# Kernel optimization log

Hardware: AMD Instinct MI355X
Metric: run time of the kernel (lower is better)

## Reference

```python
import jax, jax.numpy as jnp
import numpy as np

H = 64      # hidden_size
IN = 3      # input_size (output_size + force dim)
OUT = 2     # output_size


def setup_inputs() -> dict:
    key = jax.random.key(0)
    ks = jax.random.split(key, 8)
    B, T, PL = 1024, 512, 300
    s = 1.0 / np.sqrt(H)  # pytorch default init range
    x = jax.random.normal(ks[0], (B, T, IN), jnp.float32)
    force = jax.random.normal(ks[1], (B, PL - 1, 1), jnp.float32)
    W_ih = jax.random.uniform(ks[2], (4 * H, IN), jnp.float32, -s, s)
    W_hh = jax.random.uniform(ks[3], (4 * H, H), jnp.float32, -s, s)
    b_ih = jax.random.uniform(ks[4], (4 * H,), jnp.float32, -s, s)
    b_hh = jax.random.uniform(ks[5], (4 * H,), jnp.float32, -s, s)
    W_out = jax.random.uniform(ks[6], (OUT, H), jnp.float32, -s, s)
    b_out = jax.random.uniform(ks[7], (OUT,), jnp.float32, -s, s)
    return {"x": x, "force": force, "W_ih": W_ih, "W_hh": W_hh,
            "b_ih": b_ih, "b_hh": b_hh, "W_out": W_out, "b_out": b_out,
            "predict_length": PL}


def _lstm_cell(h, c, x_t, W_ih, W_hh, b):
    # pytorch gate order: i, f, g, o
    g = x_t @ W_ih.T + h @ W_hh.T + b
    i, f, gg, o = jnp.split(g, 4, axis=-1)
    c_new = jax.nn.sigmoid(f) * c + jax.nn.sigmoid(i) * jnp.tanh(gg)
    h_new = jax.nn.sigmoid(o) * jnp.tanh(c_new)
    return h_new, c_new


def reference(x, force, W_ih, W_hh, b_ih, b_hh, W_out, b_out, predict_length):
    b = b_ih + b_hh
    B = x.shape[0]
    h0 = jnp.zeros((B, H), x.dtype)
    c0 = jnp.zeros((B, H), x.dtype)

    # ---- encoder: run LSTM over full input sequence ----
    def enc_step(carry, x_t):
        h, c = carry
        h, c = _lstm_cell(h, c, x_t, W_ih, W_hh, b)
        return (h, c), h
    (h, c), _ = jax.lax.scan(enc_step, (h0, c0), jnp.swapaxes(x, 0, 1))

    # first decoder output = out(last encoder hidden)
    y0 = h @ W_out.T + b_out  # [B, OUT]

    def dec_step(carry, f_t):
        h, c, y = carry
        x_t = jnp.concatenate([y, f_t], axis=-1)  # [B, OUT+1] == [B, IN]
        h, c = _lstm_cell(h, c, x_t, W_ih, W_hh, b)
        y = h @ W_out.T + b_out
        return (h, c, y), y
    f_seq = jnp.swapaxes(force, 0, 1)[: predict_length - 1]  # [PL-1, B, 1]
    _, ys = jax.lax.scan(dec_step, (h, c, y0), f_seq)  # [PL-1, B, OUT]

    out = jnp.concatenate([y0[:, None, :], jnp.swapaxes(ys, 0, 1)], axis=1)
    return out  # [B, predict_length, OUT]
```

## Files before the change

### kernel.cpp

```cpp
#include <hip/hip_runtime.h>

#define Hh 64
#define INPUT 3
#define OUTD 2
#define BATCH 1024
#define TENC 512
#define PLEN 300

#define LOG2E 1.44269504088896340736f

__device__ __forceinline__ float tanh_(float x) {
    float t = __builtin_amdgcn_exp2f(x * (2.0f * LOG2E));
    return fmaf(-2.0f, __builtin_amdgcn_rcpf(1.0f + t), 1.0f);
}

#define QUADB(dst, src, pat)                                                   \
    dst = __int_as_float(__builtin_amdgcn_update_dpp(                          \
        0, __float_as_int(src), (pat), 0xF, 0xF, true))

#define MACQ(W, K)                                                             \
    {                                                                          \
        const float4 hv = *reinterpret_cast<const float4*>(&hb[(K)]);          \
        acc0 = fmaf((W).x, hv.x, acc0);                                        \
        acc1 = fmaf((W).y, hv.y, acc1);                                        \
        acc0 = fmaf((W).z, hv.z, acc0);                                        \
        acc1 = fmaf((W).w, hv.w, acc1);                                        \
    }

#define PIN4(W) asm volatile("" : "+v"((W).x), "+v"((W).y), "+v"((W).z), "+v"((W).w))

__global__ __launch_bounds__(256, 4)
void lstm_forecast_kernel(const float* __restrict__ x,
                          const float* __restrict__ force,
                          const float* __restrict__ W_ih,
                          const float* __restrict__ W_hh,
                          const float* __restrict__ b_ih,
                          const float* __restrict__ b_hh,
                          const float* __restrict__ W_out,
                          const float* __restrict__ b_out,
                          float* __restrict__ out)
{
    const int b    = blockIdx.x;
    const int tid  = threadIdx.x;
    const int u    = tid >> 2;
    const int g    = tid & 3;
    const int wv   = tid >> 6;
    const int lane = tid & 63;
    const int r    = (g << 6) + u;

    __shared__ __align__(16) float x_s[TENC * INPUT];
    __shared__ __align__(16) float f_s[PLEN - 1];
    __shared__ __align__(16) float h_s[2][Hh];
    __shared__ __align__(16) float y_s[2][8];

    const float* xb = x + (size_t)b * (TENC * INPUT);
    for (int i = tid; i < TENC * INPUT; i += 256) x_s[i] = xb[i];
    const float* fb = force + (size_t)b * (PLEN - 1);
    for (int i = tid; i < PLEN - 1; i += 256) f_s[i] = fb[i];
    if (tid < Hh) h_s[0][tid] = 0.0f;

    const float4* wrow = reinterpret_cast<const float4*>(W_hh + (size_t)r * Hh);
    float4 w0 = wrow[0],  w1 = wrow[1],  w2 = wrow[2],  w3 = wrow[3];
    float4 w4 = wrow[4],  w5 = wrow[5],  w6 = wrow[6],  w7 = wrow[7];
    float4 w8 = wrow[8],  w9 = wrow[9],  wA = wrow[10], wB = wrow[11];
    float4 wC = wrow[12], wD = wrow[13], wE = wrow[14], wF = wrow[15];
    PIN4(w0); PIN4(w1); PIN4(w2); PIN4(w3);
    PIN4(w4); PIN4(w5); PIN4(w6); PIN4(w7);
    PIN4(w8); PIN4(w9); PIN4(wA); PIN4(wB);
    PIN4(wC); PIN4(wD); PIN4(wE); PIN4(wF);

    const float wi0  = W_ih[r * INPUT + 0];
    const float wi1  = W_ih[r * INPUT + 1];
    const float wi2  = W_ih[r * INPUT + 2];
    const float bias = b_ih[r] + b_hh[r];

    const float kmul = (g == 2) ? (-2.0f * LOG2E) : (-LOG2E);
    const float am   = (g == 2) ? 2.0f : 1.0f;
    const float acK  = (g == 2) ? -1.0f : 0.0f;

    const float wog = (g == 1) ? W_out[Hh + u] : W_out[u];
    const float bo0 = b_out[0], bo1 = b_out[1];

    float c  = 0.0f;
    int   rp = 0;

    __syncthreads();

    auto lstm_step = [&](float x0, float x1, float x2, bool do_y) {
        const float* hb = h_s[rp];
        float acc0 = fmaf(wi0, x0, bias);
        float acc1 = fmaf(wi1, x1, 0.0f);
        acc0 = fmaf(wi2, x2, acc0);
        MACQ(w0, 0)  MACQ(w1, 4)  MACQ(w2, 8)  MACQ(w3, 12)
        MACQ(w4, 16) MACQ(w5, 20) MACQ(w6, 24) MACQ(w7, 28)
        MACQ(w8, 32) MACQ(w9, 36) MACQ(wA, 40) MACQ(wB, 44)
        MACQ(wC, 48) MACQ(wD, 52) MACQ(wE, 56) MACQ(wF, 60)
        const float acc = acc0 + acc1;

        const float e  = __builtin_amdgcn_exp2f(acc * kmul);
        const float rr = __builtin_amdgcn_rcpf(1.0f + e);
        const float a  = fmaf(am, rr, acK);

        float gi, gf, gg, go;
        QUADB(gi, a, 0x00);
        QUADB(gf, a, 0x55);
        QUADB(gg, a, 0xAA);
        QUADB(go, a, 0xFF);

        c = fmaf(gf, c, gi * gg);
        const float h = go * tanh_(c);

        if (g == 0) h_s[rp ^ 1][u] = h;

        if (do_y) {
            float pp = (g < 2) ? wog * h : 0.0f;
            pp += __shfl_xor(pp, 4, 64);
            pp += __shfl_xor(pp, 8, 64);
            pp += __shfl_xor(pp, 16, 64);
            pp += __shfl_xor(pp, 32, 64);
            if (lane < 2) y_s[rp ^ 1][wv * 2 + lane] = pp;
        }

        rp ^= 1;
        __syncthreads();
    };

    auto read_y = [&]() -> float2 {
        const float4 ya = *reinterpret_cast<const float4*>(&y_s[rp][0]);
        const float4 yb = *reinterpret_cast<const float4*>(&y_s[rp][4]);
        return make_float2(ya.x + ya.z + yb.x + yb.z + bo0,
                           ya.y + ya.w + yb.y + yb.w + bo1);
    };

    for (int t = 0; t < TENC - 1; ++t) {
        lstm_step(x_s[3 * t + 0], x_s[3 * t + 1], x_s[3 * t + 2], false);
    }
    lstm_step(x_s[3 * (TENC - 1) + 0], x_s[3 * (TENC - 1) + 1],
              x_s[3 * (TENC - 1) + 2], true);

    float2 y = read_y();
    float* ob = out + (size_t)b * (PLEN * OUTD);
    if (tid == 0) { ob[0] = y.x; ob[1] = y.y; }

    for (int d = 0; d < PLEN - 1; ++d) {
        lstm_step(y.x, y.y, f_s[d], true);
        y = read_y();
        if (tid == 0) { ob[(d + 1) * 2 + 0] = y.x; ob[(d + 1) * 2 + 1] = y.y; }
    }
}

extern "C" void kernel_launch(void* const* d_in, const int* in_sizes, int n_in,
                              void* d_out, int out_size, void* d_ws, size_t ws_size,
                              hipStream_t stream) {
    const float* x     = (const float*)d_in[0];
    const float* force = (const float*)d_in[1];
    const float* W_ih  = (const float*)d_in[2];
    const float* W_hh  = (const float*)d_in[3];
    const float* b_ih  = (const float*)d_in[4];
    const float* b_hh  = (const float*)d_in[5];
    const float* W_out = (const float*)d_in[6];
    const float* b_out = (const float*)d_in[7];
    float* out = (float*)d_out;

    lstm_forecast_kernel<<<BATCH, 256, 0, stream>>>(
        x, force, W_ih, W_hh, b_ih, b_hh, W_out, b_out, out);
}
```

Baseline: 685.1 us.

## Process four batch elements per block, reusing register-held W_hh rows

Each 256-thread block now advances four sequences at once. Each thread's W_hh row, held in registers, is reused across four hidden-state vectors, and the grid shrinks from 1024 to 256 blocks. Inputs and forcing are transposed into shared memory so that one step's values for the four sequences are contiguous, and the thread-to-unit mapping changes so each wave owns 16 units. The aim is to amortise weight registers and barrier/latency overhead over more work per step. The cost is a fourfold longer dependent chain per step and only 256 blocks, which may underfill the GPU's compute units.

```diff
diff --git a/kernel.cpp b/kernel.cpp
--- a/kernel.cpp
+++ b/kernel.cpp
@@ -4,6 +4,7 @@
 #define INPUT 3
 #define OUTD 2
 #define BATCH 1024
+#define NB 4
 #define TENC 512
 #define PLEN 300
 
@@ -18,18 +19,23 @@
     dst = __int_as_float(__builtin_amdgcn_update_dpp(                          \
         0, __float_as_int(src), (pat), 0xF, 0xF, true))
 
-#define MACQ(W, K)                                                             \
+#define MACK(W, K)                                                             \
     {                                                                          \
-        const float4 hv = *reinterpret_cast<const float4*>(&hb[(K)]);          \
-        acc0 = fmaf((W).x, hv.x, acc0);                                        \
-        acc1 = fmaf((W).y, hv.y, acc1);                                        \
-        acc0 = fmaf((W).z, hv.z, acc0);                                        \
-        acc1 = fmaf((W).w, hv.w, acc1);                                        \
-    }
-
-#define PIN4(W) asm volatile("" : "+v"((W).x), "+v"((W).y), "+v"((W).z), "+v"((W).w))
-
-__global__ __launch_bounds__(256, 4)
+        const float4 hv0 = *reinterpret_cast<const float4*>(hb + 0 * Hh + (K));\
+        const float4 hv1 = *reinterpret_cast<const float4*>(hb + 1 * Hh + (K));\
+        const float4 hv2 = *reinterpret_cast<const float4*>(hb + 2 * Hh + (K));\
+        const float4 hv3 = *reinterpret_cast<const float4*>(hb + 3 * Hh + (K));\
+        aa0 = fmaf((W).x, hv0.x, aa0); ab0 = fmaf((W).y, hv0.y, ab0);          \
+        aa0 = fmaf((W).z, hv0.z, aa0); ab0 = fmaf((W).w, hv0.w, ab0);          \
+        aa1 = fmaf((W).x, hv1.x, aa1); ab1 = fmaf((W).y, hv1.y, ab1);          \
+        aa1 = fmaf((W).z, hv1.z, aa1); ab1 = fmaf((W).w, hv1.w, ab1);          \
+        aa2 = fmaf((W).x, hv2.x, aa2); ab2 = fmaf((W).y, hv2.y, ab2);          \
+        aa2 = fmaf((W).z, hv2.z, aa2); ab2 = fmaf((W).w, hv2.w, ab2);          \
+        aa3 = fmaf((W).x, hv3.x, aa3); ab3 = fmaf((W).y, hv3.y, ab3);          \
+        aa3 = fmaf((W).z, hv3.z, aa3); ab3 = fmaf((W).w, hv3.w, ab3);          \
+    }
+
+__global__ __launch_bounds__(256, 1)
 void lstm_forecast_kernel(const float* __restrict__ x,
                           const float* __restrict__ force,
                           const float* __restrict__ W_ih,
@@ -40,34 +46,40 @@
                           const float* __restrict__ b_out,
                           float* __restrict__ out)
 {
-    const int b    = blockIdx.x;
     const int tid  = threadIdx.x;
-    const int u    = tid >> 2;
     const int g    = tid & 3;
+    const int lane = tid & 63;
+    const int ul   = lane >> 2;
     const int wv   = tid >> 6;
-    const int lane = tid & 63;
+    const int u    = wv * 16 + ul;
     const int r    = (g << 6) + u;
-
-    __shared__ __align__(16) float x_s[TENC * INPUT];
-    __shared__ __align__(16) float f_s[PLEN - 1];
-    __shared__ __align__(16) float h_s[2][Hh];
-    __shared__ __align__(16) float y_s[2][8];
-
-    const float* xb = x + (size_t)b * (TENC * INPUT);
-    for (int i = tid; i < TENC * INPUT; i += 256) x_s[i] = xb[i];
-    const float* fb = force + (size_t)b * (PLEN - 1);
-    for (int i = tid; i < PLEN - 1; i += 256) f_s[i] = fb[i];
-    if (tid < Hh) h_s[0][tid] = 0.0f;
+    const int b0   = blockIdx.x * NB;
+
+    __shared__ __align__(16) float xc_s[TENC * INPUT * NB];
+    __shared__ __align__(16) float fc_s[(PLEN - 1) * NB];
+    __shared__ __align__(16) float h_s[2][NB * Hh];
+    __shared__ __align__(16) float y_s[2][NB][4][2];
+
+    for (int i = tid; i < TENC * INPUT * NB; i += 256) {
+        const int bb  = i / (TENC * INPUT);
+        const int rem = i - bb * (TENC * INPUT);
+        const int t   = rem / INPUT;
+        const int c_  = rem - t * INPUT;
+        xc_s[t * (INPUT * NB) + c_ * NB + bb] =
+            x[(size_t)(b0 + bb) * (TENC * INPUT) + rem];
+    }
+    for (int i = tid; i < (PLEN - 1) * NB; i += 256) {
+        const int bb = i / (PLEN - 1);
+        const int d  = i - bb * (PLEN - 1);
+        fc_s[d * NB + bb] = force[(size_t)(b0 + bb) * (PLEN - 1) + d];
+    }
+    h_s[0][tid] = 0.0f;
 
     const float4* wrow = reinterpret_cast<const float4*>(W_hh + (size_t)r * Hh);
-    float4 w0 = wrow[0],  w1 = wrow[1],  w2 = wrow[2],  w3 = wrow[3];
-    float4 w4 = wrow[4],  w5 = wrow[5],  w6 = wrow[6],  w7 = wrow[7];
-    float4 w8 = wrow[8],  w9 = wrow[9],  wA = wrow[10], wB = wrow[11];
-    float4 wC = wrow[12], wD = wrow[13], wE = wrow[14], wF = wrow[15];
-    PIN4(w0); PIN4(w1); PIN4(w2); PIN4(w3);
-    PIN4(w4); PIN4(w5); PIN4(w6); PIN4(w7);
-    PIN4(w8); PIN4(w9); PIN4(wA); PIN4(wB);
-    PIN4(wC); PIN4(wD); PIN4(wE); PIN4(wF);
+    const float4 w0 = wrow[0],  w1 = wrow[1],  w2 = wrow[2],  w3 = wrow[3];
+    const float4 w4 = wrow[4],  w5 = wrow[5],  w6 = wrow[6],  w7 = wrow[7];
+    const float4 w8 = wrow[8],  w9 = wrow[9],  wA = wrow[10], wB = wrow[11];
+    const float4 wC = wrow[12], wD = wrow[13], wE = wrow[14], wF = wrow[15];
 
     const float wi0  = W_ih[r * INPUT + 0];
     const float wi1  = W_ih[r * INPUT + 1];
@@ -81,71 +93,113 @@
     const float wog = (g == 1) ? W_out[Hh + u] : W_out[u];
     const float bo0 = b_out[0], bo1 = b_out[1];
 
-    float c  = 0.0f;
+    float c0 = 0.0f, c1 = 0.0f, c2 = 0.0f, c3 = 0.0f;
     int   rp = 0;
 
     __syncthreads();
 
-    auto lstm_step = [&](float x0, float x1, float x2, bool do_y) {
+    auto lstm_step = [&](float4 xc0, float4 xc1, float4 xc2, bool do_y) {
         const float* hb = h_s[rp];
-        float acc0 = fmaf(wi0, x0, bias);
-        float acc1 = fmaf(wi1, x1, 0.0f);
-        acc0 = fmaf(wi2, x2, acc0);
-        MACQ(w0, 0)  MACQ(w1, 4)  MACQ(w2, 8)  MACQ(w3, 12)
-        MACQ(w4, 16) MACQ(w5, 20) MACQ(w6, 24) MACQ(w7, 28)
-        MACQ(w8, 32) MACQ(w9, 36) MACQ(wA, 40) MACQ(wB, 44)
-        MACQ(wC, 48) MACQ(wD, 52) MACQ(wE, 56) MACQ(wF, 60)
-        const float acc = acc0 + acc1;
-
-        const float e  = __builtin_amdgcn_exp2f(acc * kmul);
-        const float rr = __builtin_amdgcn_rcpf(1.0f + e);
-        const float a  = fmaf(am, rr, acK);
-
-        float gi, gf, gg, go;
-        QUADB(gi, a, 0x00);
-        QUADB(gf, a, 0x55);
-        QUADB(gg, a, 0xAA);
-        QUADB(go, a, 0xFF);
-
-        c = fmaf(gf, c, gi * gg);
-        const float h = go * tanh_(c);
-
-        if (g == 0) h_s[rp ^ 1][u] = h;
+        float aa0 = fmaf(wi0, xc0.x, bias);
+        float aa1 = fmaf(wi0, xc0.y, bias);
+        float aa2 = fmaf(wi0, xc0.z, bias);
+        float aa3 = fmaf(wi0, xc0.w, bias);
+        float ab0 = wi1 * xc1.x, ab1 = wi1 * xc1.y;
+        float ab2 = wi1 * xc1.z, ab3 = wi1 * xc1.w;
+        aa0 = fmaf(wi2, xc2.x, aa0); aa1 = fmaf(wi2, xc2.y, aa1);
+        aa2 = fmaf(wi2, xc2.z, aa2); aa3 = fmaf(wi2, xc2.w, aa3);
+
+        MACK(w0, 0)  MACK(w1, 4)  MACK(w2, 8)  MACK(w3, 12)
+        MACK(w4, 16) MACK(w5, 20) MACK(w6, 24) MACK(w7, 28)
+        MACK(w8, 32) MACK(w9, 36) MACK(wA, 40) MACK(wB, 44)
+        MACK(wC, 48) MACK(wD, 52) MACK(wE, 56) MACK(wF, 60)
+
+        float h0, h1, h2, h3;
+        #define GATEUPD(ACC0, ACC1, CC, HH)                                    \
+        {                                                                      \
+            const float acc = (ACC0) + (ACC1);                                 \
+            const float e   = __builtin_amdgcn_exp2f(acc * kmul);              \
+            const float rr  = __builtin_amdgcn_rcpf(1.0f + e);                 \
+            const float a   = fmaf(am, rr, acK);                               \
+            float gi, gf, gg, go;                                              \
+            QUADB(gi, a, 0x00); QUADB(gf, a, 0x55);                            \
+            QUADB(gg, a, 0xAA); QUADB(go, a, 0xFF);                            \
+            CC = fmaf(gf, CC, gi * gg);                                        \
+            HH = go * tanh_(CC);                                               \
+        }
+        GATEUPD(aa0, ab0, c0, h0)
+        GATEUPD(aa1, ab1, c1, h1)
+        GATEUPD(aa2, ab2, c2, h2)
+        GATEUPD(aa3, ab3, c3, h3)
+        #undef GATEUPD
+
+        const float hw = (g == 0) ? h0 : (g == 1) ? h1 : (g == 2) ? h2 : h3;
+        h_s[rp ^ 1][(g << 6) + u] = hw;
 
         if (do_y) {
-            float pp = (g < 2) ? wog * h : 0.0f;
-            pp += __shfl_xor(pp, 4, 64);
-            pp += __shfl_xor(pp, 8, 64);
-            pp += __shfl_xor(pp, 16, 64);
-            pp += __shfl_xor(pp, 32, 64);
-            if (lane < 2) y_s[rp ^ 1][wv * 2 + lane] = pp;
-        }
-
+            float p0 = (g < 2) ? wog * h0 : 0.0f;
+            float p1 = (g < 2) ? wog * h1 : 0.0f;
+            float p2 = (g < 2) ? wog * h2 : 0.0f;
+            float p3 = (g < 2) ? wog * h3 : 0.0f;
+            #pragma unroll
+            for (int m = 4; m <= 32; m <<= 1) {
+                p0 += __shfl_xor(p0, m, 64);
+                p1 += __shfl_xor(p1, m, 64);
+                p2 += __shfl_xor(p2, m, 64);
+                p3 += __shfl_xor(p3, m, 64);
+            }
+            if (g < 2 && ul < NB) {
+                const float pw = (ul == 0) ? p0 : (ul == 1) ? p1
+                               : (ul == 2) ? p2 : p3;
+                y_s[rp ^ 1][ul][wv][g] = pw;
+            }
+        }
         rp ^= 1;
         __syncthreads();
     };
 
-    auto read_y = [&]() -> float2 {
-        const float4 ya = *reinterpret_cast<const float4*>(&y_s[rp][0]);
-        const float4 yb = *reinterpret_cast<const float4*>(&y_s[rp][4]);
-        return make_float2(ya.x + ya.z + yb.x + yb.z + bo0,
-                           ya.y + ya.w + yb.y + yb.w + bo1);
+    float4 yv0, yv1;
+    auto read_y = [&]() {
+        #define RDY(B, O0, O1)                                                 \
+        {                                                                      \
+            const float4 q0 = *reinterpret_cast<const float4*>(&y_s[rp][B][0][0]);\
+            const float4 q1 = *reinterpret_cast<const float4*>(&y_s[rp][B][2][0]);\
+            O0 = q0.x + q0.z + q1.x + q1.z + bo0;                              \
+            O1 = q0.y + q0.w + q1.y + q1.w + bo1;                              \
+        }
+        RDY(0, yv0.x, yv1.x) RDY(1, yv0.y, yv1.y)
+        RDY(2, yv0.z, yv1.z) RDY(3, yv0.w, yv1.w)
+        #undef RDY
     };
 
-    for (int t = 0; t < TENC - 1; ++t) {
-        lstm_step(x_s[3 * t + 0], x_s[3 * t + 1], x_s[3 * t + 2], false);
-    }
-    lstm_step(x_s[3 * (TENC - 1) + 0], x_s[3 * (TENC - 1) + 1],
-              x_s[3 * (TENC - 1) + 2], true);
-
-    float2 y = read_y();
-    float* ob = out + (size_t)b * (PLEN * OUTD);
-    if (tid == 0) { ob[0] = y.x; ob[1] = y.y; }
+    for (int t = 0; t < TENC; ++t) {
+        const float* xp = xc_s + t * (INPUT * NB);
+        const float4 xc0 = *reinterpret_cast<const float4*>(xp + 0);
+        const float4 xc1 = *reinterpret_cast<const float4*>(xp + NB);
+        const float4 xc2 = *reinterpret_cast<const float4*>(xp + 2 * NB);
+        lstm_step(xc0, xc1, xc2, t == TENC - 1);
+    }
+
+    float* ob = out + (size_t)b0 * (PLEN * OUTD);
 
     for (int d = 0; d < PLEN - 1; ++d) {
-        lstm_step(y.x, y.y, f_s[d], true);
-        y = read_y();
-        if (tid == 0) { ob[(d + 1) * 2 + 0] = y.x; ob[(d + 1) * 2 + 1] = y.y; }
+        read_y();
+        if (tid == 0) {
+            *reinterpret_cast<float2*>(ob + 0 * (PLEN * OUTD) + d * 2) = make_float2(yv0.x, yv1.x);
+            *reinterpret_cast<float2*>(ob + 1 * (PLEN * OUTD) + d * 2) = make_float2(yv0.y, yv1.y);
+            *reinterpret_cast<float2*>(ob + 2 * (PLEN * OUTD) + d * 2) = make_float2(yv0.z, yv1.z);
+            *reinterpret_cast<float2*>(ob + 3 * (PLEN * OUTD) + d * 2) = make_float2(yv0.w, yv1.w);
+        }
+        const float4 fc = *reinterpret_cast<const float4*>(fc_s + d * NB);
+        lstm_step(yv0, yv1, fc, true);
+    }
+    read_y();
+    if (tid == 0) {
+        const int d = PLEN - 1;
+        *reinterpret_cast<float2*>(ob + 0 * (PLEN * OUTD) + d * 2) = make_float2(yv0.x, yv1.x);
+        *reinterpret_cast<float2*>(ob + 1 * (PLEN * OUTD) + d * 2) = make_float2(yv0.y, yv1.y);
+        *reinterpret_cast<float2*>(ob + 2 * (PLEN * OUTD) + d * 2) = make_float2(yv0.z, yv1.z);
+        *reinterpret_cast<float2*>(ob + 3 * (PLEN * OUTD) + d * 2) = make_float2(yv0.w, yv1.w);
     }
 }
 
@@ -162,6 +216,6 @@
     const float* b_out = (const float*)d_in[7];
     float* out = (float*)d_out;
 
-    lstm_forecast_kernel<<<BATCH, 256, 0, stream>>>(
+    lstm_forecast_kernel<<<BATCH / NB, 256, 0, stream>>>(
         x, force, W_ih, W_hh, b_ih, b_hh, W_out, b_out, out);
 }
```

Measured after the change: 1.170 ms. 70.8% more time.

## Split each gate row across two lanes and process two batch rows per block

Applied to the files above, without the earlier changes.

Each block now handles two batch sequences with 512 threads. Each W_hh row is split across two lanes that each hold 32 weights, and the two halves are combined with a ds_swizzle xor. Both sequences' cells run between a single barrier per timestep, which halves the number of barriers per sequence and shortens each thread's dot-product chain. The costs are an extra swizzle reduction, more threads per block, and the two sequences' work being serialized inside each thread.

```diff
diff --git a/kernel.cpp b/kernel.cpp
--- a/kernel.cpp
+++ b/kernel.cpp
@@ -4,32 +4,33 @@
 #define INPUT 3
 #define OUTD 2
 #define BATCH 1024
+#define NB 2
 #define TENC 512
 #define PLEN 300
 
 #define LOG2E 1.44269504088896340736f
 
+__device__ __forceinline__ float exp2_(float x) { return __builtin_amdgcn_exp2f(x); }
+__device__ __forceinline__ float rcp_(float x)  { return __builtin_amdgcn_rcpf(x); }
 __device__ __forceinline__ float tanh_(float x) {
-    float t = __builtin_amdgcn_exp2f(x * (2.0f * LOG2E));
-    return fmaf(-2.0f, __builtin_amdgcn_rcpf(1.0f + t), 1.0f);
+    float t = exp2_(x * (2.0f * LOG2E));
+    return fmaf(-2.0f, rcp_(1.0f + t), 1.0f);
 }
 
 #define QUADB(dst, src, pat)                                                   \
     dst = __int_as_float(__builtin_amdgcn_update_dpp(                          \
         0, __float_as_int(src), (pat), 0xF, 0xF, true))
 
-#define MACQ(W, K)                                                             \
+#define SWZ_XOR4(x) __int_as_float(__builtin_amdgcn_ds_swizzle(__float_as_int(x), 0x101F))
+
+#define MACH(W, K)                                                             \
     {                                                                          \
-        const float4 hv = *reinterpret_cast<const float4*>(&hb[(K)]);          \
-        acc0 = fmaf((W).x, hv.x, acc0);                                        \
-        acc1 = fmaf((W).y, hv.y, acc1);                                        \
-        acc0 = fmaf((W).z, hv.z, acc0);                                        \
-        acc1 = fmaf((W).w, hv.w, acc1);                                        \
+        const float4 hv = *reinterpret_cast<const float4*>(hb + (K));          \
+        a0 = fmaf((W).x, hv.x, a0); a1 = fmaf((W).y, hv.y, a1);                \
+        a0 = fmaf((W).z, hv.z, a0); a1 = fmaf((W).w, hv.w, a1);                \
     }
 
-#define PIN4(W) asm volatile("" : "+v"((W).x), "+v"((W).y), "+v"((W).z), "+v"((W).w))
-
-__global__ __launch_bounds__(256, 4)
+__global__ __launch_bounds__(512, 4)
 void lstm_forecast_kernel(const float* __restrict__ x,
                           const float* __restrict__ force,
                           const float* __restrict__ W_ih,
@@ -40,112 +41,130 @@
                           const float* __restrict__ b_out,
                           float* __restrict__ out)
 {
-    const int b    = blockIdx.x;
     const int tid  = threadIdx.x;
-    const int u    = tid >> 2;
-    const int g    = tid & 3;
+    const int lane = tid & 63;
     const int wv   = tid >> 6;
-    const int lane = tid & 63;
-    const int r    = (g << 6) + u;
+    const int g    = lane & 3;
+    const int half = (lane >> 2) & 1;
+    const int ulo  = lane >> 3;
+    const int u    = wv * 8 + ulo;
+    const int row  = (g << 6) + u;
+    const int b0   = blockIdx.x * NB;
 
-    __shared__ __align__(16) float x_s[TENC * INPUT];
-    __shared__ __align__(16) float f_s[PLEN - 1];
-    __shared__ __align__(16) float h_s[2][Hh];
-    __shared__ __align__(16) float y_s[2][8];
+    __shared__ __align__(16) float x_s[NB][TENC * 4];
+    __shared__ __align__(16) float f_s[NB][PLEN - 1];
+    __shared__ __align__(16) float h_s[2][NB][Hh];
+    __shared__ __align__(16) float y_s[2][NB][2][8];
 
-    const float* xb = x + (size_t)b * (TENC * INPUT);
-    for (int i = tid; i < TENC * INPUT; i += 256) x_s[i] = xb[i];
-    const float* fb = force + (size_t)b * (PLEN - 1);
-    for (int i = tid; i < PLEN - 1; i += 256) f_s[i] = fb[i];
-    if (tid < Hh) h_s[0][tid] = 0.0f;
+    for (int i = tid; i < TENC * INPUT * NB; i += 512) {
+        const int bb  = i / (TENC * INPUT);
+        const int rem = i - bb * (TENC * INPUT);
+        const int t   = rem / INPUT;
+        const int c_  = rem - t * INPUT;
+        x_s[bb][t * 4 + c_] = x[(size_t)(b0 + bb) * (TENC * INPUT) + rem];
+    }
+    for (int i = tid; i < (PLEN - 1) * NB; i += 512) {
+        const int bb = i / (PLEN - 1);
+        const int d  = i - bb * (PLEN - 1);
+        f_s[bb][d] = force[(size_t)(b0 + bb) * (PLEN - 1) + d];
+    }
+    if (tid < NB * Hh) h_s[0][tid >> 6][tid & 63] = 0.0f;
 
-    const float4* wrow = reinterpret_cast<const float4*>(W_hh + (size_t)r * Hh);
-    float4 w0 = wrow[0],  w1 = wrow[1],  w2 = wrow[2],  w3 = wrow[3];
-    float4 w4 = wrow[4],  w5 = wrow[5],  w6 = wrow[6],  w7 = wrow[7];
-    float4 w8 = wrow[8],  w9 = wrow[9],  wA = wrow[10], wB = wrow[11];
-    float4 wC = wrow[12], wD = wrow[13], wE = wrow[14], wF = wrow[15];
-    PIN4(w0); PIN4(w1); PIN4(w2); PIN4(w3);
-    PIN4(w4); PIN4(w5); PIN4(w6); PIN4(w7);
-    PIN4(w8); PIN4(w9); PIN4(wA); PIN4(wB);
-    PIN4(wC); PIN4(wD); PIN4(wE); PIN4(wF);
+    const float4* wr = reinterpret_cast<const float4*>(W_hh + (size_t)row * Hh + half * 32);
+    const float4 w0 = wr[0], w1 = wr[1], w2 = wr[2], w3 = wr[3];
+    const float4 w4 = wr[4], w5 = wr[5], w6 = wr[6], w7 = wr[7];
 
-    const float wi0  = W_ih[r * INPUT + 0];
-    const float wi1  = W_ih[r * INPUT + 1];
-    const float wi2  = W_ih[r * INPUT + 2];
-    const float bias = b_ih[r] + b_hh[r];
+    const float hm   = (half == 0) ? 1.0f : 0.0f;
+    const float wi0  = hm * W_ih[row * INPUT + 0];
+    const float wi1  = hm * W_ih[row * INPUT + 1];
+    const float wi2  = hm * W_ih[row * INPUT + 2];
+    const float bias = hm * (b_ih[row] + b_hh[row]);
 
     const float kmul = (g == 2) ? (-2.0f * LOG2E) : (-LOG2E);
     const float am   = (g == 2) ? 2.0f : 1.0f;
     const float acK  = (g == 2) ? -1.0f : 0.0f;
 
-    const float wog = (g == 1) ? W_out[Hh + u] : W_out[u];
+    const float wog = (g < 2 && half == 0) ? W_out[g * Hh + u] : 0.0f;
     const float bo0 = b_out[0], bo1 = b_out[1];
 
-    float c  = 0.0f;
+    float cA = 0.0f, cB = 0.0f;
     int   rp = 0;
 
     __syncthreads();
 
-    auto lstm_step = [&](float x0, float x1, float x2, bool do_y) {
-        const float* hb = h_s[rp];
-        float acc0 = fmaf(wi0, x0, bias);
-        float acc1 = fmaf(wi1, x1, 0.0f);
-        acc0 = fmaf(wi2, x2, acc0);
-        MACQ(w0, 0)  MACQ(w1, 4)  MACQ(w2, 8)  MACQ(w3, 12)
-        MACQ(w4, 16) MACQ(w5, 20) MACQ(w6, 24) MACQ(w7, 28)
-        MACQ(w8, 32) MACQ(w9, 36) MACQ(wA, 40) MACQ(wB, 44)
-        MACQ(wC, 48) MACQ(wD, 52) MACQ(wE, 56) MACQ(wF, 60)
-        const float acc = acc0 + acc1;
+    auto cell = [&](int bb, float x0, float x1, float x2, float& c, bool do_y, int ph) {
+        const float* hb = &h_s[ph][bb][half << 5];
+        float a0 = fmaf(wi0, x0, bias);
+        a0 = fmaf(wi1, x1, a0);
+        a0 = fmaf(wi2, x2, a0);
+        float a1 = 0.0f;
+        MACH(w0, 0)  MACH(w1, 4)  MACH(w2, 8)  MACH(w3, 12)
+        MACH(w4, 16) MACH(w5, 20) MACH(w6, 24) MACH(w7, 28)
+        float p = a0 + a1;
+        p += SWZ_XOR4(p);
 
-        const float e  = __builtin_amdgcn_exp2f(acc * kmul);
-        const float rr = __builtin_amdgcn_rcpf(1.0f + e);
+        const float e  = exp2_(p * kmul);
+        const float rr = rcp_(1.0f + e);
         const float a  = fmaf(am, rr, acK);
 
         float gi, gf, gg, go;
-        QUADB(gi, a, 0x00);
-        QUADB(gf, a, 0x55);
-        QUADB(gg, a, 0xAA);
-        QUADB(go, a, 0xFF);
+        QUADB(gi, a, 0x00); QUADB(gf, a, 0x55);
+        QUADB(gg, a, 0xAA); QUADB(go, a, 0xFF);
 
         c = fmaf(gf, c, gi * gg);
         const float h = go * tanh_(c);
 
-        if (g == 0) h_s[rp ^ 1][u] = h;
+        if ((lane & 7) == 0) h_s[ph ^ 1][bb][u] = h;
 
         if (do_y) {
-            float pp = (g < 2) ? wog * h : 0.0f;
-            pp += __shfl_xor(pp, 4, 64);
-            pp += __shfl_xor(pp, 8, 64);
-            pp += __shfl_xor(pp, 16, 64);
-            pp += __shfl_xor(pp, 32, 64);
-            if (lane < 2) y_s[rp ^ 1][wv * 2 + lane] = pp;
+            float yp = wog * h;
+            yp += __shfl_xor(yp, 8, 64);
+            yp += __shfl_xor(yp, 16, 64);
+            yp += __shfl_xor(yp, 32, 64);
+            if (g < 2 && half == 0 && ulo == 0) y_s[ph ^ 1][bb][g][wv] = yp;
         }
-
-        rp ^= 1;
-        __syncthreads();
     };
 
-    auto read_y = [&]() -> float2 {
-        const float4 ya = *reinterpret_cast<const float4*>(&y_s[rp][0]);
-        const float4 yb = *reinterpret_cast<const float4*>(&y_s[rp][4]);
-        return make_float2(ya.x + ya.z + yb.x + yb.z + bo0,
-                           ya.y + ya.w + yb.y + yb.w + bo1);
+    auto assemble = [&](int bb, int ph) -> float2 {
+        const float4 q0 = *reinterpret_cast<const float4*>(&y_s[ph][bb][0][0]);
+        const float4 q1 = *reinterpret_cast<const float4*>(&y_s[ph][bb][0][4]);
+        const float4 q2 = *reinterpret_cast<const float4*>(&y_s[ph][bb][1][0]);
+        const float4 q3 = *reinterpret_cast<const float4*>(&y_s[ph][bb][1][4]);
+        return make_float2(q0.x + q0.y + q0.z + q0.w + q1.x + q1.y + q1.z + q1.w + bo0,
+                           q2.x + q2.y + q2.z + q2.w + q3.x + q3.y + q3.z + q3.w + bo1);
     };
 
-    for (int t = 0; t < TENC - 1; ++t) {
-        lstm_step(x_s[3 * t + 0], x_s[3 * t + 1], x_s[3 * t + 2], false);
+    for (int t = 0; t < TENC; ++t) {
+        const float4 xa = *reinterpret_cast<const float4*>(&x_s[0][t * 4]);
+        const float4 xb = *reinterpret_cast<const float4*>(&x_s[1][t * 4]);
+        const bool dy = (t == TENC - 1);
+        cell(0, xa.x, xa.y, xa.z, cA, dy, rp);
+        cell(1, xb.x, xb.y, xb.z, cB, dy, rp);
+        __syncthreads();
+        rp ^= 1;
     }
-    lstm_step(x_s[3 * (TENC - 1) + 0], x_s[3 * (TENC - 1) + 1],
-              x_s[3 * (TENC - 1) + 2], true);
-
-    float2 y = read_y();
-    float* ob = out + (size_t)b * (PLEN * OUTD);
-    if (tid == 0) { ob[0] = y.x; ob[1] = y.y; }
 
     for (int d = 0; d < PLEN - 1; ++d) {
-        lstm_step(y.x, y.y, f_s[d], true);
-        y = read_y();
-        if (tid == 0) { ob[(d + 1) * 2 + 0] = y.x; ob[(d + 1) * 2 + 1] = y.y; }
+        const float2 yA = assemble(0, rp);
+        const float2 yB = assemble(1, rp);
+        if (tid < 2) {
+            const float2 v = (tid == 0) ? yA : yB;
+            *reinterpret_cast<float2*>(out + (size_t)(b0 + tid) * (PLEN * OUTD) + d * OUTD) = v;
+        }
+        const float fA = f_s[0][d];
+        const float fB = f_s[1][d];
+        cell(0, yA.x, yA.y, fA, cA, true, rp);
+        cell(1, yB.x, yB.y, fB, cB, true, rp);
+        __syncthreads();
+        rp ^= 1;
+    }
+    {
+        const float2 yA = assemble(0, rp);
+        const float2 yB = assemble(1, rp);
+        if (tid < 2) {
+            const float2 v = (tid == 0) ? yA : yB;
+            *reinterpret_cast<float2*>(out + (size_t)(b0 + tid) * (PLEN * OUTD) + (PLEN - 1) * OUTD) = v;
+        }
     }
 }
 
@@ -162,6 +181,6 @@
     const float* b_out = (const float*)d_in[7];
     float* out = (float*)d_out;
 
-    lstm_forecast_kernel<<<BATCH, 256, 0, stream>>>(
+    lstm_forecast_kernel<<<BATCH / NB, 512, 0, stream>>>(
         x, force, W_ih, W_hh, b_ih, b_hh, W_out, b_out, out);
 }
```

Result: slower. 975.3 us (+42.4%).
